# Kernel optimization log

Hardware: AMD Instinct MI355X
Metric: run time of the kernel (lower is better)

Reference implementation:

```python
import jax, jax.numpy as jnp
import numpy as np

DIM = 1024
N_HEADS = 16
HEAD_DIM = DIM // N_HEADS


def setup_inputs() -> dict:
    key = jax.random.key(0)
    ks = jax.random.split(key, 7)
    B, S = 2, 2048
    scale = 0.02
    return {
        "q": jax.random.normal(ks[0], (B, S, DIM), dtype=jnp.float32),
        "k": jax.random.normal(ks[1], (B, S, DIM), dtype=jnp.float32),
        "v": jax.random.normal(ks[2], (B, S, DIM), dtype=jnp.float32),
        # torch nn.Linear weights are [out_features, in_features]; y = x @ W.T
        "wq": jax.random.normal(ks[3], (DIM, DIM), dtype=jnp.float32) * scale,
        "wk": jax.random.normal(ks[4], (DIM, DIM), dtype=jnp.float32) * scale,
        "wv": jax.random.normal(ks[5], (DIM, DIM), dtype=jnp.float32) * scale,
        "wo": jax.random.normal(ks[6], (DIM, DIM), dtype=jnp.float32) * scale,
    }


def reference(q, k, v, wq, wk, wv, wo):
    B, S, _ = q.shape
    H, D = N_HEADS, HEAD_DIM
    # projections (torch Linear: x @ W.T), reshape to [B, H, S, D]
    xq = (q @ wq.T).reshape(B, S, H, D).transpose(0, 2, 1, 3)
    xk = (k @ wk.T).reshape(B, S, H, D).transpose(0, 2, 1, 3)
    xv = (v @ wv.T).reshape(B, S, H, D).transpose(0, 2, 1, 3)
    # scaled dot-product attention with causal mask
    scores = jnp.einsum("bhqd,bhkd->bhqk", xq, xk) / jnp.sqrt(jnp.float32(D))
    causal = jnp.tril(jnp.ones((S, S), dtype=bool))
    scores = jnp.where(causal, scores, -jnp.inf)
    attn = jax.nn.softmax(scores.astype(jnp.float32), axis=-1).astype(xq.dtype)
    # dropout prob = 0.0 (eval-mode / deterministic reference)
    out = jnp.einsum("bhqk,bhkd->bhqd", attn, xv)
    out = out.transpose(0, 2, 1, 3).reshape(B, S, H * D)
    return out @ wo.T
```

## Files before the change

kernel.cpp:

```cpp
#include <hip/hip_runtime.h>
#include <hip/hip_bf16.h>
#include <stdint.h>


typedef short s16x8 __attribute__((ext_vector_type(8)));
typedef float f32x4 __attribute__((ext_vector_type(4)));

#define MFMA_BF16 __builtin_amdgcn_mfma_f32_16x16x32_bf16

static __device__ __forceinline__ unsigned short f2bf(float f) {
    union { float f; unsigned u; } x{f};
    unsigned r = x.u + 0x7fff + ((x.u >> 16) & 1);
    return (unsigned short)(r >> 16);
}
static __device__ __forceinline__ unsigned pk2h(float a, float b) {
    __hip_bfloat162 h = __float22bfloat162_rn(float2{a, b});
    return *(unsigned*)&h;
}

static __device__ __forceinline__ void ald16(unsigned short* lds, const unsigned short* g) {
    __builtin_amdgcn_global_load_lds(
        (const __attribute__((address_space(1))) unsigned int*)g,
        (__attribute__((address_space(3))) unsigned int*)lds, 16, 0, 0);
}

#define QSCL 0.18033688f

__global__ __launch_bounds__(256) void convert_all_kernel(
        const float* __restrict__ q, const float* __restrict__ k,
        const float* __restrict__ v,
        const float* __restrict__ wq, const float* __restrict__ wk,
        const float* __restrict__ wv, const float* __restrict__ wo,
        unsigned short* __restrict__ dst) {
    const size_t idx = ((size_t)blockIdx.x * 256 + threadIdx.x) * 8;
    const int region = (int)(idx >> 22);
    const float* src;
    size_t off;
    if (region == 0)      { src = q; off = idx; }
    else if (region == 1) { src = k; off = idx & 4194303; }
    else if (region == 2) { src = v; off = idx & 4194303; }
    else {
        const int wsel = (int)((idx >> 20) & 3);
        src = wsel == 0 ? wq : wsel == 1 ? wk : wsel == 2 ? wv : wo;
        off = idx & 1048575;
    }
    const float4* p = (const float4*)(src + off);
    float4 a = p[0], b = p[1];
    uint4 u;
    u.x = pk2h(a.x, a.y); u.y = pk2h(a.z, a.w);
    u.z = pk2h(b.x, b.y); u.w = pk2h(b.z, b.w);
    *(uint4*)(dst + idx) = u;
}

__global__ __launch_bounds__(256) void wconvert_kernel(
        const float* __restrict__ wq, const float* __restrict__ wk,
        const float* __restrict__ wv, const float* __restrict__ wo,
        unsigned short* __restrict__ Wb) {
    const size_t idx = ((size_t)blockIdx.x * 256 + threadIdx.x) * 8;
    const int region = (int)(idx >> 20);
    const size_t off = idx & 1048575;
    const float* src = region == 0 ? wq : region == 1 ? wk : region == 2 ? wv : wo;
    const float4* p = (const float4*)(src + off);
    float4 a = p[0], b = p[1];
    uint4 u;
    u.x = pk2h(a.x, a.y); u.y = pk2h(a.z, a.w);
    u.z = pk2h(b.x, b.y); u.w = pk2h(b.z, b.w);
    *(uint4*)(Wb + idx) = u;
}

__global__ __launch_bounds__(256) void proj3b_kernel(
        const unsigned short* __restrict__ Qb, const unsigned short* __restrict__ Kb,
        const unsigned short* __restrict__ Vb, const unsigned short* __restrict__ Wb,
        unsigned short* __restrict__ Xq, unsigned short* __restrict__ Xk,
        unsigned short* __restrict__ Xvt) {
    constexpr int Kd = 1024;
    __shared__ union {
        struct { unsigned short A[3][128 * 32]; unsigned short B[3][128 * 32]; } s;
        unsigned short T[4 * 64 * 68];
    } sm;

    const int z = blockIdx.z;
    const unsigned short* A  = z == 0 ? Qb : z == 1 ? Kb : Vb;
    const unsigned short* Bw = Wb + (size_t)z * 1048576;

    const int t = threadIdx.x;
    const int m0 = blockIdx.x * 128, n0 = blockIdx.y * 128;
    const int w = t >> 6, lane = t & 63, fr = lane & 15, g = lane >> 4;
    const int wm = (w >> 1) * 64, wn = (w & 1) * 64;
    const int brow = t >> 2;
    const int cB = (t & 3) ^ ((t >> 3) & 3);
    const int sB = g ^ ((fr >> 1) & 3);

    f32x4 acc[4][4] = {};

    auto STAGE = [&](int p, int kk) {
        ald16(sm.s.A[p] + (size_t)w * 512,        A  + (size_t)(m0 + brow) * Kd + kk + cB * 8);
        ald16(sm.s.A[p] + 2048 + (size_t)w * 512, A  + (size_t)(m0 + 64 + brow) * Kd + kk + cB * 8);
        ald16(sm.s.B[p] + (size_t)w * 512,        Bw + (size_t)(n0 + brow) * Kd + kk + cB * 8);
        ald16(sm.s.B[p] + 2048 + (size_t)w * 512, Bw + (size_t)(n0 + 64 + brow) * Kd + kk + cB * 8);
    };

    STAGE(0, 0);
    STAGE(1, 32);
    int bi = 0, nb = 2;

    for (int k0 = 0; k0 < Kd; k0 += 32) {
        if (k0 < Kd - 64) {
            STAGE(nb, k0 + 64);
            asm volatile("s_waitcnt vmcnt(8)" ::: "memory");
        } else if (k0 < Kd - 32) {
            asm volatile("s_waitcnt vmcnt(4)" ::: "memory");
        } else {
            asm volatile("s_waitcnt vmcnt(0)" ::: "memory");
        }
        __builtin_amdgcn_s_barrier();
        asm volatile("" ::: "memory");

        s16x8 af[4], bfv[4];
#pragma unroll
        for (int mi = 0; mi < 4; ++mi)
            af[mi] = *(const s16x8*)(sm.s.A[bi] + (wm + mi * 16 + fr) * 32 + sB * 8);
#pragma unroll
        for (int ni = 0; ni < 4; ++ni)
            bfv[ni] = *(const s16x8*)(sm.s.B[bi] + (wn + ni * 16 + fr) * 32 + sB * 8);
#pragma unroll
        for (int mi = 0; mi < 4; ++mi)
#pragma unroll
            for (int ni = 0; ni < 4; ++ni)
                acc[mi][ni] = MFMA_BF16(af[mi], bfv[ni], acc[mi][ni], 0, 0, 0);

        asm volatile("" ::: "memory");
        __builtin_amdgcn_s_barrier();
        bi = bi == 2 ? 0 : bi + 1;
        nb = nb == 2 ? 0 : nb + 1;
    }

    if (z != 2) {
        unsigned short* C = z ? Xk : Xq;
        const float osc = z == 0 ? QSCL : 1.0f;
#pragma unroll
        for (int mi = 0; mi < 4; ++mi)
#pragma unroll
            for (int ni = 0; ni < 4; ++ni)
#pragma unroll
                for (int reg = 0; reg < 4; ++reg)
                    C[(size_t)(m0 + wm + mi * 16 + g * 4 + reg) * 1024 +
                      n0 + wn + ni * 16 + fr] = f2bf(acc[mi][ni][reg] * osc);
    } else {
        unsigned short* T = sm.T + w * (64 * 68);
#pragma unroll
        for (int mi = 0; mi < 4; ++mi)
#pragma unroll
            for (int ni = 0; ni < 4; ++ni) {
                uint2 u;
                u.x = pk2h(acc[mi][ni][0], acc[mi][ni][1]);
                u.y = pk2h(acc[mi][ni][2], acc[mi][ni][3]);
                *(uint2*)(T + (ni * 16 + fr) * 68 + mi * 16 + g * 4) = u;
            }
        __asm__ __volatile__("" ::: "memory");
#pragma unroll
        for (int pass = 0; pass < 8; ++pass) {
            const int row = pass * 8 + (lane >> 3);
            const int chk = lane & 7;
            uint4 d = *(const uint4*)(T + row * 68 + chk * 8);
            *(uint4*)(Xvt + (size_t)(n0 + wn + row) * 4096 + m0 + wm + chk * 8) = d;
        }
    }
}

__global__ __launch_bounds__(256) void proj3_kernel(
        const float* __restrict__ q, const float* __restrict__ k, const float* __restrict__ v,
        const unsigned short* __restrict__ Wb,
        unsigned short* __restrict__ Xq, unsigned short* __restrict__ Xk,
        unsigned short* __restrict__ Xvt) {
    constexpr int Kd = 1024;
    __shared__ unsigned short lsA[128 * 40];
    __shared__ unsigned short lsB[128 * 32];
    __shared__ unsigned short Tls[4 * 64 * 68];

    const int z = blockIdx.z;
    const float* A = z == 0 ? q : z == 1 ? k : v;
    const unsigned short* Bw = Wb + (size_t)z * 1048576;

    const int t = threadIdx.x;
    const int m0 = blockIdx.x * 128, n0 = blockIdx.y * 128;
    const int w = t >> 6, lane = t & 63, fr = lane & 15, g = lane >> 4, fq = g * 8;
    const int wm = (w >> 1) * 64, wn = (w & 1) * 64;
    const int ar = t >> 1, ac = (t & 1) * 16;
    const int brow = t >> 2;
    const int cB = (t & 3) ^ ((t >> 3) & 3);
    const int sB = g ^ ((fr >> 1) & 3);

    f32x4 acc[4][4] = {};

    for (int k0 = 0; k0 < Kd; k0 += 32) {
        ald16(lsB + (size_t)w * 512,        Bw + (size_t)(n0 + brow) * Kd + k0 + cB * 8);
        ald16(lsB + 2048 + (size_t)w * 512, Bw + (size_t)(n0 + 64 + brow) * Kd + k0 + cB * 8);
        {
            const float4* pa = (const float4*)(A + (size_t)(m0 + ar) * Kd + k0 + ac);
            float4 a0 = pa[0], a1 = pa[1], a2 = pa[2], a3 = pa[3];
            uint4 u0, u1;
            u0.x = pk2h(a0.x, a0.y); u0.y = pk2h(a0.z, a0.w);
            u0.z = pk2h(a1.x, a1.y); u0.w = pk2h(a1.z, a1.w);
            u1.x = pk2h(a2.x, a2.y); u1.y = pk2h(a2.z, a2.w);
            u1.z = pk2h(a3.x, a3.y); u1.w = pk2h(a3.z, a3.w);
            *(uint4*)(lsA + ar * 40 + ac)     = u0;
            *(uint4*)(lsA + ar * 40 + ac + 8) = u1;
        }
        __syncthreads();

        s16x8 af[4], bfv[4];
#pragma unroll
        for (int mi = 0; mi < 4; ++mi)
            af[mi] = *(const s16x8*)(lsA + (wm + mi * 16 + fr) * 40 + fq);
#pragma unroll
        for (int ni = 0; ni < 4; ++ni)
            bfv[ni] = *(const s16x8*)(lsB + (wn + ni * 16 + fr) * 32 + sB * 8);
#pragma unroll
        for (int mi = 0; mi < 4; ++mi)
#pragma unroll
            for (int ni = 0; ni < 4; ++ni)
                acc[mi][ni] = MFMA_BF16(af[mi], bfv[ni], acc[mi][ni], 0, 0, 0);
        __syncthreads();
    }

    if (z != 2) {
        unsigned short* C = z ? Xk : Xq;
        const float osc = z == 0 ? QSCL : 1.0f;
#pragma unroll
        for (int mi = 0; mi < 4; ++mi)
#pragma unroll
            for (int ni = 0; ni < 4; ++ni)
#pragma unroll
                for (int reg = 0; reg < 4; ++reg)
                    C[(size_t)(m0 + wm + mi * 16 + g * 4 + reg) * 1024 +
                      n0 + wn + ni * 16 + fr] = f2bf(acc[mi][ni][reg] * osc);
    } else {
        unsigned short* T = Tls + w * (64 * 68);
#pragma unroll
        for (int mi = 0; mi < 4; ++mi)
#pragma unroll
            for (int ni = 0; ni < 4; ++ni) {
                uint2 u;
                u.x = pk2h(acc[mi][ni][0], acc[mi][ni][1]);
                u.y = pk2h(acc[mi][ni][2], acc[mi][ni][3]);
                *(uint2*)(T + (ni * 16 + fr) * 68 + mi * 16 + g * 4) = u;
            }
        __asm__ __volatile__("" ::: "memory");
#pragma unroll
        for (int pass = 0; pass < 8; ++pass) {
            const int row = pass * 8 + (lane >> 3);
            const int chk = lane & 7;
            uint4 d = *(const uint4*)(T + row * 68 + chk * 8);
            *(uint4*)(Xvt + (size_t)(n0 + wn + row) * 4096 + m0 + wm + chk * 8) = d;
        }
    }
}

static __device__ __forceinline__ void slab_tail(
        const f32x4 sf[4], int kt, int qt, int qrow, float& l_part,
        f32x4* oacc, unsigned short* Pw, const s16x8 vf[4][2], int fr, int g) {
    float e[4][4];
    const bool diag = (kt == qt);
#pragma unroll
    for (int m16 = 0; m16 < 4; ++m16)
#pragma unroll
        for (int r = 0; r < 4; ++r) {
            float x = sf[m16][r];
            if (diag) {
                const int keyg = kt * 64 + m16 * 16 + g * 4 + r;
                x = (keyg <= qrow) ? x : -1e30f;
            }
            const float ee = __builtin_amdgcn_exp2f(x);
            e[m16][r] = ee;
            l_part += ee;
        }
#pragma unroll
    for (int m16 = 0; m16 < 4; ++m16) {
        uint2 u;
        u.x = pk2h(e[m16][0], e[m16][1]);
        u.y = pk2h(e[m16][2], e[m16][3]);
        const int ch = 2 * m16 + (g >> 1);
        *(uint2*)(Pw + fr * 64 + ((ch ^ (fr & 7)) * 8) + (g & 1) * 4) = u;
    }
    __asm__ __volatile__("" ::: "memory");
    s16x8 pf0 = *(const s16x8*)(Pw + fr * 64 + ((g ^ (fr & 7)) * 8));
    s16x8 pf1 = *(const s16x8*)(Pw + fr * 64 + (((4 + g) ^ (fr & 7)) * 8));
#pragma unroll
    for (int m16 = 0; m16 < 4; ++m16) {
        oacc[m16] = MFMA_BF16(vf[m16][0], pf0, oacc[m16], 0, 0, 0);
        oacc[m16] = MFMA_BF16(vf[m16][1], pf1, oacc[m16], 0, 0, 0);
    }
    __asm__ __volatile__("" ::: "memory");
}

__global__ __launch_bounds__(256, 4) void flash_attn_kernel(
        const unsigned short* __restrict__ Xq, const unsigned short* __restrict__ Xk,
        const unsigned short* __restrict__ Xvt, unsigned short* __restrict__ Oa) {
    __shared__ unsigned short Kls[2][64 * 64];
    __shared__ unsigned short Vls[2][64 * 64];
    __shared__ unsigned short Pls[4][16 * 64];

    const int t = threadIdx.x;
    const int bh = blockIdx.x;
    const int qt = 31 - blockIdx.y;
    const int b = bh >> 4, h = bh & 15;
    const size_t rbase = (size_t)b * 2048;
    const int cbase = h * 64;

    const int w = t >> 6, lane = t & 63, fr = lane & 15, g = lane >> 4, fq = g * 8;
    const int qrow = qt * 64 + w * 16 + fr;

    const unsigned short* qp = Xq + (rbase + qrow) * 1024 + cbase;
    s16x8 qf0 = *(const s16x8*)(qp + fq);
    s16x8 qf1 = *(const s16x8*)(qp + 32 + fq);

    float l = 0.f;
    f32x4 o[4] = {};

    const int r0 = w * 16 + (lane >> 3), r1 = r0 + 8;
    const int s8 = lane & 7;
    const int c0 = s8 ^ (r0 & 7), c1 = s8 ^ (r1 & 7);
    const unsigned short* kbase = Xk + rbase * 1024 + cbase;
    const size_t vrow0 = (size_t)(cbase + r0) * 4096 + rbase + c0 * 8;
    const size_t vrow1 = (size_t)(cbase + r1) * 4096 + rbase + c1 * 8;

    uint4 kA = *(const uint4*)(kbase + (size_t)r0 * 1024 + c0 * 8);
    uint4 kB = *(const uint4*)(kbase + (size_t)r1 * 1024 + c1 * 8);
    uint4 vA = *(const uint4*)(Xvt + vrow0);
    uint4 vB = *(const uint4*)(Xvt + vrow1);

    *(uint4*)(Kls[0] + (w * 16) * 64 + lane * 8)     = kA;
    *(uint4*)(Kls[0] + (w * 16 + 8) * 64 + lane * 8) = kB;
    *(uint4*)(Vls[0] + (w * 16) * 64 + lane * 8)     = vA;
    *(uint4*)(Vls[0] + (w * 16 + 8) * 64 + lane * 8) = vB;
    __syncthreads();

    for (int kt = 0; kt <= qt; ++kt) {
        const int cur = kt & 1;

        if (kt < qt) {
            const unsigned short* ks = kbase + (size_t)(kt + 1) * 65536;
            kA = *(const uint4*)(ks + (size_t)r0 * 1024 + c0 * 8);
            kB = *(const uint4*)(ks + (size_t)r1 * 1024 + c1 * 8);
            vA = *(const uint4*)(Xvt + vrow0 + (size_t)(kt + 1) * 64);
            vB = *(const uint4*)(Xvt + vrow1 + (size_t)(kt + 1) * 64);
        }

        s16x8 kf[4][2], vf[4][2];
#pragma unroll
        for (int m16 = 0; m16 < 4; ++m16) {
            const int rr = m16 * 16 + fr;
            kf[m16][0] = *(const s16x8*)(Kls[cur] + rr * 64 + ((g ^ (fr & 7)) * 8));
            kf[m16][1] = *(const s16x8*)(Kls[cur] + rr * 64 + (((4 + g) ^ (fr & 7)) * 8));
            vf[m16][0] = *(const s16x8*)(Vls[cur] + rr * 64 + ((g ^ (fr & 7)) * 8));
            vf[m16][1] = *(const s16x8*)(Vls[cur] + rr * 64 + (((4 + g) ^ (fr & 7)) * 8));
        }

        f32x4 s[4];
#pragma unroll
        for (int m16 = 0; m16 < 4; ++m16) {
            f32x4 zz = {};
            zz = MFMA_BF16(kf[m16][0], qf0, zz, 0, 0, 0);
            s[m16] = MFMA_BF16(kf[m16][1], qf1, zz, 0, 0, 0);
        }
        slab_tail(s, kt, qt, qrow, l, o, &Pls[w][0], vf, fr, g);

        if (kt < qt) {
            const int nxt = cur ^ 1;
            *(uint4*)(Kls[nxt] + (w * 16) * 64 + lane * 8)     = kA;
            *(uint4*)(Kls[nxt] + (w * 16 + 8) * 64 + lane * 8) = kB;
            *(uint4*)(Vls[nxt] + (w * 16) * 64 + lane * 8)     = vA;
            *(uint4*)(Vls[nxt] + (w * 16 + 8) * 64 + lane * 8) = vB;
            __syncthreads();
        }
    }

    l += __shfl_xor(l, 16, 64);
    l += __shfl_xor(l, 32, 64);
    const float inv = 1.0f / l;
#pragma unroll
    for (int m16 = 0; m16 < 4; ++m16) {
        uint2 u;
        u.x = pk2h(o[m16][0] * inv, o[m16][1] * inv);
        u.y = pk2h(o[m16][2] * inv, o[m16][3] * inv);
        *(uint2*)(Oa + (rbase + qrow) * 1024 + cbase + m16 * 16 + g * 4) = u;
    }
}

__global__ __launch_bounds__(256) void outproj_kernel(
        const unsigned short* __restrict__ Oa, const unsigned short* __restrict__ Wo,
        float* __restrict__ out) {
    constexpr int Kd = 1024;
    __shared__ unsigned short lsA[3][64 * 32];
    __shared__ unsigned short lsB[3][128 * 32];

    const int t = threadIdx.x;
    const int m0 = blockIdx.x * 64, n0 = blockIdx.y * 128;
    const int w = t >> 6, lane = t & 63, fr = lane & 15, g = lane >> 4;
    const int wm = (w >> 1) * 32, wn = (w & 1) * 64;
    const int brow = t >> 2;
    const int cB = (t & 3) ^ ((t >> 3) & 3);
    const int sB = g ^ ((fr >> 1) & 3);

    f32x4 acc[2][4] = {};

    auto STAGE = [&](int p, int kk) {
        ald16(lsA[p] + (size_t)w * 512,        Oa + (size_t)(m0 + brow) * Kd + kk + cB * 8);
        ald16(lsB[p] + (size_t)w * 512,        Wo + (size_t)(n0 + brow) * Kd + kk + cB * 8);
        ald16(lsB[p] + 2048 + (size_t)w * 512, Wo + (size_t)(n0 + 64 + brow) * Kd + kk + cB * 8);
    };

    STAGE(0, 0);
    STAGE(1, 32);
    int bi = 0, nb = 2;

    for (int k0 = 0; k0 < Kd; k0 += 32) {
        if (k0 < Kd - 64) {
            STAGE(nb, k0 + 64);
            asm volatile("s_waitcnt vmcnt(6)" ::: "memory");
        } else if (k0 < Kd - 32) {
            asm volatile("s_waitcnt vmcnt(3)" ::: "memory");
        } else {
            asm volatile("s_waitcnt vmcnt(0)" ::: "memory");
        }
        __builtin_amdgcn_s_barrier();
        asm volatile("" ::: "memory");

        s16x8 af[2], bfv[4];
#pragma unroll
        for (int mi = 0; mi < 2; ++mi)
            af[mi] = *(const s16x8*)(lsA[bi] + (wm + mi * 16 + fr) * 32 + sB * 8);
#pragma unroll
        for (int ni = 0; ni < 4; ++ni)
            bfv[ni] = *(const s16x8*)(lsB[bi] + (wn + ni * 16 + fr) * 32 + sB * 8);
#pragma unroll
        for (int mi = 0; mi < 2; ++mi)
#pragma unroll
            for (int ni = 0; ni < 4; ++ni)
                acc[mi][ni] = MFMA_BF16(af[mi], bfv[ni], acc[mi][ni], 0, 0, 0);

        asm volatile("" ::: "memory");
        __builtin_amdgcn_s_barrier();
        bi = bi == 2 ? 0 : bi + 1;
        nb = nb == 2 ? 0 : nb + 1;
    }

#pragma unroll
    for (int mi = 0; mi < 2; ++mi)
#pragma unroll
        for (int ni = 0; ni < 4; ++ni)
#pragma unroll
            for (int reg = 0; reg < 4; ++reg)
                out[(size_t)(m0 + wm + mi * 16 + g * 4 + reg) * 1024 +
                    n0 + wn + ni * 16 + fr] = acc[mi][ni][reg];
}

extern "C" void kernel_launch(void* const* d_in, const int* in_sizes, int n_in,
                              void* d_out, int out_size, void* d_ws, size_t ws_size,
                              hipStream_t stream) {
    const float* q  = (const float*)d_in[0];
    const float* k  = (const float*)d_in[1];
    const float* v  = (const float*)d_in[2];
    const float* wq = (const float*)d_in[3];
    const float* wk = (const float*)d_in[4];
    const float* wv = (const float*)d_in[5];
    const float* wo = (const float*)d_in[6];
    float* out = (float*)d_out;

    if (ws_size >= (size_t)64 * 1024 * 1024) {
        unsigned short* base = (unsigned short*)d_ws;
        unsigned short* Qb  = base;
        unsigned short* Kb  = base + 4194304;
        unsigned short* Vb  = base + 8388608;
        unsigned short* Wb  = base + 12582912;
        unsigned short* Xq  = base + 16777216;
        unsigned short* Xk  = base + 20971520;
        unsigned short* Xvt = base + 25165824;
        unsigned short* Oa  = base + 29360128;

        convert_all_kernel<<<8192, 256, 0, stream>>>(q, k, v, wq, wk, wv, wo, base);
        proj3b_kernel<<<dim3(32, 8, 3), 256, 0, stream>>>(Qb, Kb, Vb, Wb, Xq, Xk, Xvt);
        flash_attn_kernel<<<dim3(32, 32), 256, 0, stream>>>(Xq, Xk, Xvt, Oa);
        outproj_kernel<<<dim3(64, 8), 256, 0, stream>>>(Oa, Wb + 3145728, out);
    } else {
        unsigned short* Wb  = (unsigned short*)d_ws;
        unsigned short* Xq  = Wb  + 4194304;
        unsigned short* Xk  = Xq  + 4194304;
        unsigned short* Xvt = Xk  + 4194304;
        unsigned short* Oa  = Xvt + 4194304;

        wconvert_kernel<<<2048, 256, 0, stream>>>(wq, wk, wv, wo, Wb);
        proj3_kernel<<<dim3(32, 8, 3), 256, 0, stream>>>(q, k, v, Wb, Xq, Xk, Xvt);
        flash_attn_kernel<<<dim3(32, 32), 256, 0, stream>>>(Xq, Xk, Xvt, Oa);
        outproj_kernel<<<dim3(64, 8), 256, 0, stream>>>(Oa, Wb + 3145728, out);
    }
}
```

Before: 200.3 us.

## Pair causal query tiles per 512-thread block and split heavy tile's KV range

Flash attention blocks now process a light query tile (j) and a heavy tile (31-j) together with 8 waves. The heavy tile's remaining KV steps are split between two wave groups, and the partial outputs and row sums are merged through a union'd LDS buffer. This balances causal work across blocks and halves the grid. It also adds s_setprio around the MFMAs and restructures the outproj pipeline into a double buffer of 64-wide K stages. The cost is extra barriers, merge overhead, and higher register and LDS pressure at 512 threads.

```diff
diff --git a/kernel.cpp b/kernel.cpp
--- a/kernel.cpp
+++ b/kernel.cpp
@@ -286,105 +286,196 @@
     __asm__ __volatile__("" ::: "memory");
     s16x8 pf0 = *(const s16x8*)(Pw + fr * 64 + ((g ^ (fr & 7)) * 8));
     s16x8 pf1 = *(const s16x8*)(Pw + fr * 64 + (((4 + g) ^ (fr & 7)) * 8));
+    __builtin_amdgcn_s_setprio(1);
 #pragma unroll
     for (int m16 = 0; m16 < 4; ++m16) {
         oacc[m16] = MFMA_BF16(vf[m16][0], pf0, oacc[m16], 0, 0, 0);
         oacc[m16] = MFMA_BF16(vf[m16][1], pf1, oacc[m16], 0, 0, 0);
     }
+    __builtin_amdgcn_s_setprio(0);
     __asm__ __volatile__("" ::: "memory");
 }
 
-__global__ __launch_bounds__(256, 4) void flash_attn_kernel(
+__global__ __launch_bounds__(512, 4) void flash_attn_kernel(
         const unsigned short* __restrict__ Xq, const unsigned short* __restrict__ Xk,
         const unsigned short* __restrict__ Xvt, unsigned short* __restrict__ Oa) {
-    __shared__ unsigned short Kls[2][64 * 64];
-    __shared__ unsigned short Vls[2][64 * 64];
-    __shared__ unsigned short Pls[4][16 * 64];
+    __shared__ union {
+        struct { unsigned short K[2][64 * 64]; unsigned short V[2][64 * 64]; } s;
+        float M[4][64][20];
+    } kv;
+    __shared__ unsigned short Pls[8][16 * 64];
 
     const int t = threadIdx.x;
     const int bh = blockIdx.x;
-    const int qt = 31 - blockIdx.y;
+    const int j = blockIdx.y;
     const int b = bh >> 4, h = bh & 15;
     const size_t rbase = (size_t)b * 2048;
     const int cbase = h * 64;
 
     const int w = t >> 6, lane = t & 63, fr = lane & 15, g = lane >> 4, fq = g * 8;
-    const int qrow = qt * 64 + w * 16 + fr;
-
-    const unsigned short* qp = Xq + (rbase + qrow) * 1024 + cbase;
-    s16x8 qf0 = *(const s16x8*)(qp + fq);
-    s16x8 qf1 = *(const s16x8*)(qp + 32 + fq);
-
-    float l = 0.f;
-    f32x4 o[4] = {};
-
-    const int r0 = w * 16 + (lane >> 3), r1 = r0 + 8;
-    const int s8 = lane & 7;
-    const int c0 = s8 ^ (r0 & 7), c1 = s8 ^ (r1 & 7);
+    const int wg = w & 3;
+    const bool up = w >= 4;
+    const int qtH = 31 - j, qtL = j;
+    const int qt1 = up ? qtL : qtH;
+    const int qrow1 = qt1 * 64 + wg * 16 + fr;
+    const int qrowH = qtH * 64 + wg * 16 + fr;
+
+    {
+        const unsigned short* qp = Xq + (rbase + qrow1) * 1024 + cbase;
+    }
+    const unsigned short* qp1 = Xq + (rbase + qrow1) * 1024 + cbase;
+    s16x8 qa = *(const s16x8*)(qp1 + fq);
+    s16x8 qb = *(const s16x8*)(qp1 + 32 + fq);
+
+    float l1 = 0.f, l2 = 0.f;
+    f32x4 o1[4] = {}, o2[4] = {};
+
     const unsigned short* kbase = Xk + rbase * 1024 + cbase;
-    const size_t vrow0 = (size_t)(cbase + r0) * 4096 + rbase + c0 * 8;
-    const size_t vrow1 = (size_t)(cbase + r1) * 4096 + rbase + c1 * 8;
-
-    uint4 kA = *(const uint4*)(kbase + (size_t)r0 * 1024 + c0 * 8);
-    uint4 kB = *(const uint4*)(kbase + (size_t)r1 * 1024 + c1 * 8);
-    uint4 vA = *(const uint4*)(Xvt + vrow0);
-    uint4 vB = *(const uint4*)(Xvt + vrow1);
-
-    *(uint4*)(Kls[0] + (w * 16) * 64 + lane * 8)     = kA;
-    *(uint4*)(Kls[0] + (w * 16 + 8) * 64 + lane * 8) = kB;
-    *(uint4*)(Vls[0] + (w * 16) * 64 + lane * 8)     = vA;
-    *(uint4*)(Vls[0] + (w * 16 + 8) * 64 + lane * 8) = vB;
+
+    const int pr = w * 8 + (lane >> 3);
+    const int pc = (lane & 7) ^ (pr & 7);
+    const size_t koff1 = (size_t)pr * 1024 + pc * 8;
+    const size_t voff1 = (size_t)(cbase + pr) * 4096 + rbase + pc * 8;
+    const int pdst = pr * 64 + (lane & 7) * 8;
+
+    uint4 kR = *(const uint4*)(kbase + koff1);
+    uint4 vR = *(const uint4*)(Xvt + voff1);
+    *(uint4*)(kv.s.K[0] + pdst) = kR;
+    *(uint4*)(kv.s.V[0] + pdst) = vR;
     __syncthreads();
 
-    for (int kt = 0; kt <= qt; ++kt) {
+#define READ_FRAGS(slot) do {                                                 \
+    _Pragma("unroll")                                                         \
+    for (int m_ = 0; m_ < 4; ++m_) {                                          \
+        const int rr_ = m_ * 16 + fr;                                         \
+        kf[m_][0] = *(const s16x8*)(kv.s.K[slot] + rr_ * 64 + ((g ^ (fr & 7)) * 8));        \
+        kf[m_][1] = *(const s16x8*)(kv.s.K[slot] + rr_ * 64 + (((4 + g) ^ (fr & 7)) * 8));  \
+        vf[m_][0] = *(const s16x8*)(kv.s.V[slot] + rr_ * 64 + ((g ^ (fr & 7)) * 8));        \
+        vf[m_][1] = *(const s16x8*)(kv.s.V[slot] + rr_ * 64 + (((4 + g) ^ (fr & 7)) * 8));  \
+    } } while (0)
+
+#define SCOMPUTE(sv) do {                                                     \
+    __builtin_amdgcn_s_setprio(1);                                            \
+    _Pragma("unroll")                                                         \
+    for (int m_ = 0; m_ < 4; ++m_) {                                          \
+        f32x4 zz = {};                                                        \
+        zz = MFMA_BF16(kf[m_][0], qa, zz, 0, 0, 0);                           \
+        sv[m_] = MFMA_BF16(kf[m_][1], qb, zz, 0, 0, 0);                       \
+    }                                                                         \
+    __builtin_amdgcn_s_setprio(0); } while (0)
+
+    for (int kt = 0; kt <= qtL; ++kt) {
         const int cur = kt & 1;
-
-        if (kt < qt) {
-            const unsigned short* ks = kbase + (size_t)(kt + 1) * 65536;
-            kA = *(const uint4*)(ks + (size_t)r0 * 1024 + c0 * 8);
-            kB = *(const uint4*)(ks + (size_t)r1 * 1024 + c1 * 8);
-            vA = *(const uint4*)(Xvt + vrow0 + (size_t)(kt + 1) * 64);
-            vB = *(const uint4*)(Xvt + vrow1 + (size_t)(kt + 1) * 64);
-        }
+        kR = *(const uint4*)(kbase + (size_t)(kt + 1) * 65536 + koff1);
+        vR = *(const uint4*)(Xvt + voff1 + (size_t)(kt + 1) * 64);
 
         s16x8 kf[4][2], vf[4][2];
-#pragma unroll
-        for (int m16 = 0; m16 < 4; ++m16) {
-            const int rr = m16 * 16 + fr;
-            kf[m16][0] = *(const s16x8*)(Kls[cur] + rr * 64 + ((g ^ (fr & 7)) * 8));
-            kf[m16][1] = *(const s16x8*)(Kls[cur] + rr * 64 + (((4 + g) ^ (fr & 7)) * 8));
-            vf[m16][0] = *(const s16x8*)(Vls[cur] + rr * 64 + ((g ^ (fr & 7)) * 8));
-            vf[m16][1] = *(const s16x8*)(Vls[cur] + rr * 64 + (((4 + g) ^ (fr & 7)) * 8));
-        }
-
-        f32x4 s[4];
-#pragma unroll
-        for (int m16 = 0; m16 < 4; ++m16) {
-            f32x4 zz = {};
-            zz = MFMA_BF16(kf[m16][0], qf0, zz, 0, 0, 0);
-            s[m16] = MFMA_BF16(kf[m16][1], qf1, zz, 0, 0, 0);
-        }
-        slab_tail(s, kt, qt, qrow, l, o, &Pls[w][0], vf, fr, g);
-
-        if (kt < qt) {
-            const int nxt = cur ^ 1;
-            *(uint4*)(Kls[nxt] + (w * 16) * 64 + lane * 8)     = kA;
-            *(uint4*)(Kls[nxt] + (w * 16 + 8) * 64 + lane * 8) = kB;
-            *(uint4*)(Vls[nxt] + (w * 16) * 64 + lane * 8)     = vA;
-            *(uint4*)(Vls[nxt] + (w * 16 + 8) * 64 + lane * 8) = vB;
-            __syncthreads();
-        }
-    }
-
-    l += __shfl_xor(l, 16, 64);
-    l += __shfl_xor(l, 32, 64);
-    const float inv = 1.0f / l;
+        READ_FRAGS(cur);
+        f32x4 sv[4];
+        SCOMPUTE(sv);
+        slab_tail(sv, kt, qt1, qrow1, l1, o1, &Pls[w][0], vf, fr, g);
+
+        const int nxt = cur ^ 1;
+        *(uint4*)(kv.s.K[nxt] + pdst) = kR;
+        *(uint4*)(kv.s.V[nxt] + pdst) = vR;
+        __syncthreads();
+    }
+
+    const int base = qtL + 1;
+    const int E = base & 1;
+    const int steps = 16 - j;
+
+    if (up) {
+        const unsigned short* qpH = Xq + (rbase + qrowH) * 1024 + cbase;
+        qa = *(const s16x8*)(qpH + fq);
+        qb = *(const s16x8*)(qpH + 32 + fq);
+    }
+
+    const int r0 = wg * 16 + (lane >> 3), r1 = r0 + 8;
+    const int c0 = (lane & 7) ^ (r0 & 7), c1 = (lane & 7) ^ (r1 & 7);
+    const size_t koffA = (size_t)r0 * 1024 + c0 * 8;
+    const size_t koffB = (size_t)r1 * 1024 + c1 * 8;
+    const size_t voffA = (size_t)(cbase + r0) * 4096 + rbase + c0 * 8;
+    const size_t voffB = (size_t)(cbase + r1) * 4096 + rbase + c1 * 8;
+    const int d0 = r0 * 64 + (lane & 7) * 8;
+    const int d1 = r1 * 64 + (lane & 7) * 8;
+
+    if (up && base + 1 <= qtH) {
+        const size_t kb = (size_t)(base + 1) * 65536;
+        uint4 a0 = *(const uint4*)(kbase + kb + koffA);
+        uint4 a1 = *(const uint4*)(kbase + kb + koffB);
+        uint4 b0 = *(const uint4*)(Xvt + voffA + (size_t)(base + 1) * 64);
+        uint4 b1 = *(const uint4*)(Xvt + voffB + (size_t)(base + 1) * 64);
+        *(uint4*)(kv.s.K[E ^ 1] + d0) = a0;
+        *(uint4*)(kv.s.K[E ^ 1] + d1) = a1;
+        *(uint4*)(kv.s.V[E ^ 1] + d0) = b0;
+        *(uint4*)(kv.s.V[E ^ 1] + d1) = b1;
+    }
+    __syncthreads();
+
+    for (int s = 0; s < steps; ++s) {
+        const int mykt = base + 2 * s + (up ? 1 : 0);
+        const int slot = up ? (E ^ 1) : E;
+        const bool valid = mykt <= qtH;
+
+        s16x8 kf[4][2], vf[4][2];
+        if (valid) READ_FRAGS(slot);
+
+        const int nkt = mykt + 2;
+        const bool pf = (s + 1 < steps) && (nkt <= qtH);
+        uint4 sk0, sk1, sv0, sv1;
+        if (pf) {
+            const size_t kb = (size_t)nkt * 65536;
+            sk0 = *(const uint4*)(kbase + kb + koffA);
+            sk1 = *(const uint4*)(kbase + kb + koffB);
+            sv0 = *(const uint4*)(Xvt + voffA + (size_t)nkt * 64);
+            sv1 = *(const uint4*)(Xvt + voffB + (size_t)nkt * 64);
+        }
+        asm volatile("s_waitcnt lgkmcnt(0)" ::: "memory");
+        __builtin_amdgcn_sched_barrier(0);
+        __builtin_amdgcn_s_barrier();
+
+        if (valid) {
+            f32x4 sv[4];
+            SCOMPUTE(sv);
+            if (up) slab_tail(sv, mykt, qtH, qrowH, l2, o2, &Pls[w][0], vf, fr, g);
+            else    slab_tail(sv, mykt, qtH, qrowH, l1, o1, &Pls[w][0], vf, fr, g);
+        }
+        if (pf) {
+            *(uint4*)(kv.s.K[slot] + d0) = sk0;
+            *(uint4*)(kv.s.K[slot] + d1) = sk1;
+            *(uint4*)(kv.s.V[slot] + d0) = sv0;
+            *(uint4*)(kv.s.V[slot] + d1) = sv1;
+        }
+        asm volatile("s_waitcnt lgkmcnt(0)" ::: "memory");
+        __builtin_amdgcn_s_barrier();
+    }
+#undef READ_FRAGS
+#undef SCOMPUTE
+
+    if (up) {
+#pragma unroll
+        for (int m16 = 0; m16 < 4; ++m16)
+            *(f32x4*)&kv.M[wg][lane][m16 * 4] = o2[m16];
+        kv.M[wg][lane][16] = l2;
+    }
+    __syncthreads();
+    if (!up) {
+#pragma unroll
+        for (int m16 = 0; m16 < 4; ++m16)
+            o1[m16] += *(const f32x4*)&kv.M[wg][lane][m16 * 4];
+        l1 += kv.M[wg][lane][16];
+    }
+
+    l1 += __shfl_xor(l1, 16, 64);
+    l1 += __shfl_xor(l1, 32, 64);
+    const float inv = 1.0f / l1;
 #pragma unroll
     for (int m16 = 0; m16 < 4; ++m16) {
         uint2 u;
-        u.x = pk2h(o[m16][0] * inv, o[m16][1] * inv);
-        u.y = pk2h(o[m16][2] * inv, o[m16][3] * inv);
-        *(uint2*)(Oa + (rbase + qrow) * 1024 + cbase + m16 * 16 + g * 4) = u;
+        u.x = pk2h(o1[m16][0] * inv, o1[m16][1] * inv);
+        u.y = pk2h(o1[m16][2] * inv, o1[m16][3] * inv);
+        *(uint2*)(Oa + (rbase + qrow1) * 1024 + cbase + m16 * 16 + g * 4) = u;
     }
 }
 
@@ -392,8 +483,8 @@
         const unsigned short* __restrict__ Oa, const unsigned short* __restrict__ Wo,
         float* __restrict__ out) {
     constexpr int Kd = 1024;
-    __shared__ unsigned short lsA[3][64 * 32];
-    __shared__ unsigned short lsB[3][128 * 32];
+    __shared__ unsigned short lsA[2][2][64 * 32];
+    __shared__ unsigned short lsB[2][2][128 * 32];
 
     const int t = threadIdx.x;
     const int m0 = blockIdx.x * 64, n0 = blockIdx.y * 128;
@@ -406,44 +497,47 @@
     f32x4 acc[2][4] = {};
 
     auto STAGE = [&](int p, int kk) {
-        ald16(lsA[p] + (size_t)w * 512,        Oa + (size_t)(m0 + brow) * Kd + kk + cB * 8);
-        ald16(lsB[p] + (size_t)w * 512,        Wo + (size_t)(n0 + brow) * Kd + kk + cB * 8);
-        ald16(lsB[p] + 2048 + (size_t)w * 512, Wo + (size_t)(n0 + 64 + brow) * Kd + kk + cB * 8);
+#pragma unroll
+        for (int sub = 0; sub < 2; ++sub) {
+            const int ks = kk + sub * 32;
+            ald16(lsA[p][sub] + (size_t)w * 512,        Oa + (size_t)(m0 + brow) * Kd + ks + cB * 8);
+            ald16(lsB[p][sub] + (size_t)w * 512,        Wo + (size_t)(n0 + brow) * Kd + ks + cB * 8);
+            ald16(lsB[p][sub] + 2048 + (size_t)w * 512, Wo + (size_t)(n0 + 64 + brow) * Kd + ks + cB * 8);
+        }
     };
 
     STAGE(0, 0);
-    STAGE(1, 32);
-    int bi = 0, nb = 2;
-
-    for (int k0 = 0; k0 < Kd; k0 += 32) {
-        if (k0 < Kd - 64) {
-            STAGE(nb, k0 + 64);
+    int buf = 0;
+
+    for (int it = 0; it < 16; ++it) {
+        if (it < 15) {
+            STAGE(buf ^ 1, (it + 1) * 64);
             asm volatile("s_waitcnt vmcnt(6)" ::: "memory");
-        } else if (k0 < Kd - 32) {
-            asm volatile("s_waitcnt vmcnt(3)" ::: "memory");
         } else {
             asm volatile("s_waitcnt vmcnt(0)" ::: "memory");
         }
         __builtin_amdgcn_s_barrier();
         asm volatile("" ::: "memory");
 
-        s16x8 af[2], bfv[4];
-#pragma unroll
-        for (int mi = 0; mi < 2; ++mi)
-            af[mi] = *(const s16x8*)(lsA[bi] + (wm + mi * 16 + fr) * 32 + sB * 8);
-#pragma unroll
-        for (int ni = 0; ni < 4; ++ni)
-            bfv[ni] = *(const s16x8*)(lsB[bi] + (wn + ni * 16 + fr) * 32 + sB * 8);
-#pragma unroll
-        for (int mi = 0; mi < 2; ++mi)
+#pragma unroll
+        for (int sub = 0; sub < 2; ++sub) {
+            s16x8 af[2], bfv[4];
+#pragma unroll
+            for (int mi = 0; mi < 2; ++mi)
+                af[mi] = *(const s16x8*)(lsA[buf][sub] + (wm + mi * 16 + fr) * 32 + sB * 8);
 #pragma unroll
             for (int ni = 0; ni < 4; ++ni)
-                acc[mi][ni] = MFMA_BF16(af[mi], bfv[ni], acc[mi][ni], 0, 0, 0);
+                bfv[ni] = *(const s16x8*)(lsB[buf][sub] + (wn + ni * 16 + fr) * 32 + sB * 8);
+#pragma unroll
+            for (int mi = 0; mi < 2; ++mi)
+#pragma unroll
+                for (int ni = 0; ni < 4; ++ni)
+                    acc[mi][ni] = MFMA_BF16(af[mi], bfv[ni], acc[mi][ni], 0, 0, 0);
+        }
 
         asm volatile("" ::: "memory");
         __builtin_amdgcn_s_barrier();
-        bi = bi == 2 ? 0 : bi + 1;
-        nb = nb == 2 ? 0 : nb + 1;
+        buf ^= 1;
     }
 
 #pragma unroll
@@ -481,7 +575,7 @@
 
         convert_all_kernel<<<8192, 256, 0, stream>>>(q, k, v, wq, wk, wv, wo, base);
         proj3b_kernel<<<dim3(32, 8, 3), 256, 0, stream>>>(Qb, Kb, Vb, Wb, Xq, Xk, Xvt);
-        flash_attn_kernel<<<dim3(32, 32), 256, 0, stream>>>(Xq, Xk, Xvt, Oa);
+        flash_attn_kernel<<<dim3(32, 16), 512, 0, stream>>>(Xq, Xk, Xvt, Oa);
         outproj_kernel<<<dim3(64, 8), 256, 0, stream>>>(Oa, Wb + 3145728, out);
     } else {
         unsigned short* Wb  = (unsigned short*)d_ws;
@@ -492,7 +586,7 @@
 
         wconvert_kernel<<<2048, 256, 0, stream>>>(wq, wk, wv, wo, Wb);
         proj3_kernel<<<dim3(32, 8, 3), 256, 0, stream>>>(q, k, v, Wb, Xq, Xk, Xvt);
-        flash_attn_kernel<<<dim3(32, 32), 256, 0, stream>>>(Xq, Xk, Xvt, Oa);
+        flash_attn_kernel<<<dim3(32, 16), 512, 0, stream>>>(Xq, Xk, Xvt, Oa);
         outproj_kernel<<<dim3(64, 8), 256, 0, stream>>>(Oa, Wb + 3145728, out);
     }
 }
```

Result: slower. 282.4 us (+40.9%).
